# Kernel tuning notes

Hardware: AMD Instinct MI355X
Metric: run time of the kernel (lower is better)

Reference implementation:

```python
import jax, jax.numpy as jnp
import numpy as np

EPS = 1e-12  # torch F.normalize eps
NUM_HEADS = 4
DT = 0.25
NUM_STEPS = 4


def _l2norm(x, axis=-1):
    n = jnp.sqrt(jnp.sum(x * x, axis=axis, keepdims=True))
    return x / jnp.maximum(n, EPS)


def setup_inputs() -> dict:
    key = jax.random.key(0)
    k0, k1, k2, k3, k4 = jax.random.split(key, 5)
    B, T, D = 4, 2048, 256
    z = jax.random.normal(k0, (B, T, D), dtype=jnp.float32)
    omega = jax.random.normal(k1, (1, 1, D), dtype=jnp.float32) * 0.1
    Wqk = jax.random.normal(k2, (2 * D, D), dtype=jnp.float32) * (1.0 / np.sqrt(D))
    Wout = jax.random.normal(k3, (D, D), dtype=jnp.float32) * (1.0 / np.sqrt(D))
    bout = jax.random.normal(k4, (D,), dtype=jnp.float32) * 0.01
    return {"z": z, "omega": omega, "Wqk": Wqk, "Wout": Wout, "bout": bout}


def _kuramoto(x, omega, Wqk, Wout, bout):
    # x: [B, T, D]
    B, T, D = x.shape
    hd = D // NUM_HEADS
    qk = x @ Wqk.T  # [B, T, 2D]
    q, k = jnp.split(qk, 2, axis=-1)
    q = _l2norm(q.reshape(B, T, NUM_HEADS, hd))  # cosine-normalized per head
    k = _l2norm(k.reshape(B, T, NUM_HEADS, hd))
    # coupling: [B, H, T, T] cosine similarity
    coupling = jnp.einsum("bqhd,bkhd->bhqk", q, k)
    # sin nonlinearity replaces softmax
    force = jnp.einsum("bhqk,bkhd->bqhd", jnp.sin(coupling), k).reshape(B, T, D)
    return omega + force @ Wout.T + bout


def reference(z, omega, Wqk, Wout, bout):
    def f(x):
        return _kuramoto(x, omega, Wqk, Wout, bout)

    x = z
    for _ in range(NUM_STEPS):
        x = _l2norm(x)
        k1 = f(x)
        k2 = f(x + DT / 2 * k1)
        k3 = f(x + DT / 2 * k2)
        k4 = f(x + DT * k3)
        x = x + DT / 6 * (k1 + 2 * k2 + 2 * k3 + k4)
    return _l2norm(x)
```

## Files before the change

kernel.cpp:

```cpp
#include <hip/hip_runtime.h>
#include <cmath>

#define NB 4
#define TT 2048
#define DD 256
#define NH 4
#define BT (NB*TT)

static constexpr float DT_ = 0.25f;

typedef _Float16 f16x8 __attribute__((ext_vector_type(8)));
typedef _Float16 f16x4 __attribute__((ext_vector_type(4)));
typedef float    f32x4 __attribute__((ext_vector_type(4)));

static constexpr size_t HSZ = (size_t)NB * NH * TT * 64;
static constexpr size_t FSZ = (size_t)BT * 256;

__device__ __forceinline__ void gload16(const void* g, void* l) {
    __builtin_amdgcn_global_load_lds(
        (const __attribute__((address_space(1))) void*)g,
        (__attribute__((address_space(3))) void*)l,
        16, 0, 0);
}

__global__ __launch_bounds__(256)
void split_weights(const float* __restrict__ Wqk, const float* __restrict__ Wout,
                   _Float16* __restrict__ WqkH, _Float16* __restrict__ WqkL,
                   _Float16* __restrict__ WoutH, _Float16* __restrict__ WoutL)
{
    const int idx = blockIdx.x * 256 + threadIdx.x;
    const float4 v = (idx < 32768) ? ((const float4*)Wqk)[idx]
                                   : ((const float4*)Wout)[idx - 32768];
    f16x4 h, l;
    h[0]=(_Float16)v.x; l[0]=(_Float16)(v.x-(float)h[0]);
    h[1]=(_Float16)v.y; l[1]=(_Float16)(v.y-(float)h[1]);
    h[2]=(_Float16)v.z; l[2]=(_Float16)(v.z-(float)h[2]);
    h[3]=(_Float16)v.w; l[3]=(_Float16)(v.w-(float)h[3]);
    if (idx < 32768) { ((f16x4*)WqkH)[idx] = h; ((f16x4*)WqkL)[idx] = l; }
    else { ((f16x4*)WoutH)[idx-32768] = h; ((f16x4*)WoutL)[idx-32768] = l; }
}

__global__ __launch_bounds__(256)
void comb_weights(const float* __restrict__ Wqk, const float* __restrict__ Wout,
                  const float* __restrict__ omega, const float* __restrict__ bout,
                  _Float16* __restrict__ WcombH, _Float16* __restrict__ WcombL,
                  float* __restrict__ qkob)
{
    __shared__ float qrow[256];
    __shared__ float pr[256];
    const int n = blockIdx.x;
    const int k = threadIdx.x;
    qrow[k] = Wqk[n * 256 + k];
    __syncthreads();
    float s = 0.f;
    for (int m = 0; m < 256; ++m) s = fmaf(qrow[m], Wout[m * 256 + k], s);
    const _Float16 h = (_Float16)s;
    WcombH[n * 256 + k] = h;
    WcombL[n * 256 + k] = (_Float16)(s - (float)h);
    pr[k] = (omega[k] + bout[k]) * qrow[k];
    __syncthreads();
    if (k == 0) {
        float t = 0.f;
        for (int i = 0; i < 256; ++i) t += pr[i];
        qkob[n] = t;
    }
}

__global__ __launch_bounds__(256)
void l2norm_rows(const float* __restrict__ src, float* __restrict__ dst,
                 _Float16* __restrict__ dstH, _Float16* __restrict__ dstL) {
    const int wave = threadIdx.x >> 6;
    const int lane = threadIdx.x & 63;
    const size_t row = (size_t)blockIdx.x * 4 + wave;
    float4 v = ((const float4*)(src + row * DD))[lane];
    float ss = v.x*v.x + v.y*v.y + v.z*v.z + v.w*v.w;
    #pragma unroll
    for (int off = 32; off; off >>= 1) ss += __shfl_xor(ss, off, 64);
    const float inv = 1.0f / fmaxf(sqrtf(ss), 1e-12f);
    v.x *= inv; v.y *= inv; v.z *= inv; v.w *= inv;
    ((float4*)(dst + row * DD))[lane] = v;
    if (dstH != nullptr) {
        f16x4 h, l;
        h[0]=(_Float16)v.x; l[0]=(_Float16)(v.x-(float)h[0]);
        h[1]=(_Float16)v.y; l[1]=(_Float16)(v.y-(float)h[1]);
        h[2]=(_Float16)v.z; l[2]=(_Float16)(v.z-(float)h[2]);
        h[3]=(_Float16)v.w; l[3]=(_Float16)(v.w-(float)h[3]);
        ((f16x4*)(dstH + row * DD))[lane] = h;
        ((f16x4*)(dstL + row * DD))[lane] = l;
    }
}

__global__ __launch_bounds__(256, 2)
void gemm_mfma(const _Float16* __restrict__ AH, const _Float16* __restrict__ AL,
               const _Float16* __restrict__ BH, const _Float16* __restrict__ BL,
               const float* __restrict__ Fp, float* __restrict__ FaccP,
               float* __restrict__ qkx, const float* __restrict__ qkob,
               const float* __restrict__ omega, const float* __restrict__ bout,
               const float* __restrict__ xin, float* __restrict__ xout,
               _Float16* __restrict__ Qhi, _Float16* __restrict__ Qlo,
               _Float16* __restrict__ Khi, _Float16* __restrict__ Klo,
               _Float16* __restrict__ KtrH,
               int mode, float cc, int faccm)
{
    __shared__ _Float16 Ah[128 * 64];
    __shared__ _Float16 Al[128 * 64];
    __shared__ _Float16 Bh[64 * 64];
    __shared__ _Float16 Bl[64 * 64];
    const int m0 = blockIdx.x * 128, n0 = blockIdx.y * 64;
    const int t  = threadIdx.x;
    const int w  = t >> 6;
    const int l  = t & 63;
    const int lr = l & 15;
    const int lq = l >> 4;
    const int m7 = lr & 7;
    const int rr = l >> 3;
    const int lc  = l & 7;
    const int cg  = (lc ^ rr) * 8;
    const int swd = (lc ^ rr) * 8;
    const bool yzero = (blockIdx.y == 0);

    f32x4 acc[2][4];
    #pragma unroll
    for (int s = 0; s < 2; ++s)
        #pragma unroll
        for (int nt = 0; nt < 4; ++nt) acc[s][nt] = (f32x4){0.f,0.f,0.f,0.f};

#define GSTAGE_A(K0) do { \
        _Pragma("unroll") \
        for (int a = 0; a < 4; ++a) { \
            const int rg = 8*w + 32*a; \
            gload16(AH + (size_t)(m0 + rg + rr) * 256 + (K0) + cg, &Ah[rg * 64]); \
            gload16(AL + (size_t)(m0 + rg + rr) * 256 + (K0) + cg, &Al[rg * 64]); \
        } \
    } while (0)

#define GSTAGE_B(K0) do { \
        _Pragma("unroll") \
        for (int a = 0; a < 2; ++a) { \
            const int rg = 8*w + 32*a; \
            gload16(BH + (size_t)(n0 + rg + rr) * 256 + (K0) + cg, &Bh[rg * 64]); \
            gload16(BL + (size_t)(n0 + rg + rr) * 256 + (K0) + cg, &Bl[rg * 64]); \
        } \
    } while (0)

#define FSTAGE(K0) do { \
        _Pragma("unroll") \
        for (int a = 0; a < 4; ++a) { \
            const int row = 8*w + 32*a + rr; \
            const size_t go = (size_t)(m0 + row) * 256 + (K0) + lc * 8; \
            float sv[8]; \
            { const float4 a0 = *(const float4*)(Fp + go); \
              const float4 a1 = *(const float4*)(Fp + go + 4); \
              sv[0]=a0.x; sv[1]=a0.y; sv[2]=a0.z; sv[3]=a0.w; \
              sv[4]=a1.x; sv[5]=a1.y; sv[6]=a1.z; sv[7]=a1.w; } \
            _Pragma("unroll") \
            for (int p = 1; p < 3; ++p) { \
                const float4 a0 = *(const float4*)(Fp + (size_t)p*FSZ + go); \
                const float4 a1 = *(const float4*)(Fp + (size_t)p*FSZ + go + 4); \
                sv[0]+=a0.x; sv[1]+=a0.y; sv[2]+=a0.z; sv[3]+=a0.w; \
                sv[4]+=a1.x; sv[5]+=a1.y; sv[6]+=a1.z; sv[7]+=a1.w; } \
            if (faccm == 3) { \
                const float4 f0 = *(const float4*)(FaccP + go); \
                const float4 f1 = *(const float4*)(FaccP + go + 4); \
                sv[0]+=f0.x; sv[1]+=f0.y; sv[2]+=f0.z; sv[3]+=f0.w; \
                sv[4]+=f1.x; sv[5]+=f1.y; sv[6]+=f1.z; sv[7]+=f1.w; \
            } else if (yzero) { \
                if (faccm == 1) { \
                    *(float4*)(FaccP + go)     = make_float4(sv[0], sv[1], sv[2], sv[3]); \
                    *(float4*)(FaccP + go + 4) = make_float4(sv[4], sv[5], sv[6], sv[7]); \
                } else { \
                    float4 f0 = *(const float4*)(FaccP + go); \
                    float4 f1 = *(const float4*)(FaccP + go + 4); \
                    f0.x += 2.f*sv[0]; f0.y += 2.f*sv[1]; f0.z += 2.f*sv[2]; f0.w += 2.f*sv[3]; \
                    f1.x += 2.f*sv[4]; f1.y += 2.f*sv[5]; f1.z += 2.f*sv[6]; f1.w += 2.f*sv[7]; \
                    *(float4*)(FaccP + go)     = f0; \
                    *(float4*)(FaccP + go + 4) = f1; \
                } \
            } \
            f16x8 hv, lv; \
            _Pragma("unroll") \
            for (int e = 0; e < 8; ++e) { \
                hv[e] = (_Float16)sv[e]; \
                lv[e] = (_Float16)(sv[e] - (float)hv[e]); } \
            *(f16x8*)&Ah[row * 64 + swd] = hv; \
            *(f16x8*)&Al[row * 64 + swd] = lv; \
        } \
    } while (0)

    if (mode == 0) GSTAGE_A(0); else FSTAGE(0);
    GSTAGE_B(0);
    asm volatile("s_waitcnt vmcnt(0) lgkmcnt(0)" ::: "memory");
    __builtin_amdgcn_s_barrier();
    asm volatile("" ::: "memory");

    for (int kc = 0; kc < 4; ++kc) {
        f16x8 ah[2][2], al[2][2], bh[2][4], bl[2][4];
        #pragma unroll
        for (int c = 0; c < 2; ++c) {
            const int xo = (((4*c + lq) ^ m7) << 4);
            #pragma unroll
            for (int s = 0; s < 2; ++s) {
                ah[c][s] = *(const f16x8*)((const char*)Ah + (32*w + 16*s + lr) * 128 + xo);
                al[c][s] = *(const f16x8*)((const char*)Al + (32*w + 16*s + lr) * 128 + xo);
            }
            #pragma unroll
            for (int nt = 0; nt < 4; ++nt) {
                bh[c][nt] = *(const f16x8*)((const char*)Bh + (16*nt + lr) * 128 + xo);
                bl[c][nt] = *(const f16x8*)((const char*)Bl + (16*nt + lr) * 128 + xo);
            }
        }
        asm volatile("s_waitcnt lgkmcnt(0)" ::: "memory");
        __builtin_amdgcn_s_barrier();
        asm volatile("" ::: "memory");
        if (kc < 3) {
            GSTAGE_B((kc + 1) * 64);
            if (mode == 0) GSTAGE_A((kc + 1) * 64); else FSTAGE((kc + 1) * 64);
        }
        #pragma unroll
        for (int c = 0; c < 2; ++c)
            #pragma unroll
            for (int s = 0; s < 2; ++s)
                #pragma unroll
                for (int nt = 0; nt < 4; ++nt) {
                    acc[s][nt] = __builtin_amdgcn_mfma_f32_16x16x32_f16(ah[c][s], bh[c][nt], acc[s][nt], 0, 0, 0);
                    acc[s][nt] = __builtin_amdgcn_mfma_f32_16x16x32_f16(ah[c][s], bl[c][nt], acc[s][nt], 0, 0, 0);
                    acc[s][nt] = __builtin_amdgcn_mfma_f32_16x16x32_f16(al[c][s], bh[c][nt], acc[s][nt], 0, 0, 0);
                }
        if (kc < 3) asm volatile("s_waitcnt vmcnt(0) lgkmcnt(0)" ::: "memory");
        __builtin_amdgcn_s_barrier();
        asm volatile("" ::: "memory");
    }
#undef GSTAGE_A
#undef GSTAGE_B
#undef FSTAGE

    if (mode == 2) {
        #pragma unroll
        for (int s = 0; s < 2; ++s) {
            const int row0 = m0 + 32*w + 16*s + 4*lq;
            #pragma unroll
            for (int nt = 0; nt < 4; ++nt) {
                const int col = n0 + 16*nt + lr;
                const float ob = omega[col] + bout[col];
                #pragma unroll
                for (int r = 0; r < 4; ++r) {
                    const size_t off = (size_t)(row0 + r) * 256 + col;
                    xout[off] = xin[off] + (DT_ / 6.0f) * acc[s][nt][r] + DT_ * ob;
                }
            }
        }
    } else {
        float val[2][4][4];
        #pragma unroll
        for (int s = 0; s < 2; ++s) {
            const int row0 = m0 + 32*w + 16*s + 4*lq;
            #pragma unroll
            for (int nt = 0; nt < 4; ++nt) {
                const int col = n0 + 16*nt + lr;
                #pragma unroll
                for (int r = 0; r < 4; ++r) {
                    const size_t qo = (size_t)(row0 + r) * 512 + col;
                    if (mode == 0) {
                        val[s][nt][r] = acc[s][nt][r];
                        qkx[qo] = acc[s][nt][r];
                    } else {
                        val[s][nt][r] = qkx[qo] + cc * (acc[s][nt][r] + qkob[col]);
                    }
                }
            }
        }
        float ss[2][4];
        #pragma unroll
        for (int s = 0; s < 2; ++s)
            #pragma unroll
            for (int r = 0; r < 4; ++r) {
                float v = 0.f;
                #pragma unroll
                for (int nt = 0; nt < 4; ++nt) v += val[s][nt][r] * val[s][nt][r];
                ss[s][r] = v;
            }
        #pragma unroll
        for (int off = 1; off < 16; off <<= 1)
            #pragma unroll
            for (int s = 0; s < 2; ++s)
                #pragma unroll
                for (int r = 0; r < 4; ++r)
                    ss[s][r] += __shfl_xor(ss[s][r], off, 64);
        const int  b    = m0 >> 11;
        const int  h    = (n0 >> 6) & 3;
        const bool is_k = (n0 >= 256);
        const size_t bhi = (size_t)b * NH + h;
        _Float16* dhi = (is_k ? Khi : Qhi) + bhi * (size_t)TT * 64;
        _Float16* dlo = (is_k ? Klo : Qlo) + bhi * (size_t)TT * 64;
        const int mloc = m0 & (TT - 1);
        _Float16* Pt = Ah;
        #pragma unroll
        for (int s = 0; s < 2; ++s) {
            const int r0 = 32*w + 16*s + 4*lq;
            float inv[4];
            #pragma unroll
            for (int r = 0; r < 4; ++r) inv[r] = 1.0f / fmaxf(sqrtf(ss[s][r]), 1e-12f);
            #pragma unroll
            for (int nt = 0; nt < 4; ++nt) {
                const int d = 16*nt + lr;
                f16x4 hv, lv;
                #pragma unroll
                for (int r = 0; r < 4; ++r) {
                    const float v2 = val[s][nt][r] * inv[r];
                    hv[r] = (_Float16)v2;
                    lv[r] = (_Float16)(v2 - (float)hv[r]);
                    dhi[(size_t)(mloc + r0 + r) * 64 + d] = hv[r];
                    dlo[(size_t)(mloc + r0 + r) * 64 + d] = lv[r];
                }
                if (is_k) {
                    *(f16x4*)((char*)Pt + d * 256 + ((r0 * 2) ^ ((d & 7) << 4))) = hv;
                }
            }
        }
        if (is_k) {
            __syncthreads();
            const size_t kb = bhi * (size_t)64 * TT + mloc;
            #pragma unroll
            for (int p = 0; p < 4; ++p) {
                const int d   = (t >> 4) + 16 * p;
                const int lm0 = (t & 15) * 8;
                f16x8 v = *(const f16x8*)((const char*)Pt + d * 256 + ((lm0 * 2) ^ ((d & 7) << 4)));
                *(f16x8*)(KtrH + kb + (size_t)d * TT + lm0) = v;
            }
        }
    }
}

__global__ __launch_bounds__(256, 3)
void kuramoto_attn(const _Float16* __restrict__ Qhi, const _Float16* __restrict__ Qlo,
                   const _Float16* __restrict__ Khi, const _Float16* __restrict__ Klo,
                   const _Float16* __restrict__ KtrH,
                   float* __restrict__ Fp)
{
    __shared__ _Float16 KjH[64 * 64];
    __shared__ _Float16 KjL[64 * 64];
    __shared__ _Float16 KdH[64 * 64];
    __shared__ _Float16 Pw[4][2][16 * 64];
    const int bh = blockIdx.x;
    const int b  = bh >> 2, h = bh & 3;
    const size_t base  = (size_t)bh * TT * 64;
    const size_t tbase = (size_t)bh * 64 * TT;
    const int t0 = blockIdx.y * 11;
    const int tn = (blockIdx.y == 2) ? 10 : 11;
    float* Fout = Fp + (size_t)blockIdx.y * FSZ;
    const int t = threadIdx.x;
    const int w = t >> 6;
    const int l = t & 63;
    const int lr = l & 15;
    const int lq = l >> 4;
    const int i0 = blockIdx.z * 128 + w * 32;
    const int m7 = lr & 7;
    const int x0 = ((lq ^ m7) << 4);
    const int x1 = (((lq + 4) ^ m7) << 4);
    const int rr = l >> 3;
    const int lc8 = (l & 7) * 8;
    const int sw = ((l & 7) ^ rr) * 8;
    const int rg = 8 * w + rr;

    f16x8 qh[2][2], ql[2][2];
    #pragma unroll
    for (int s = 0; s < 2; ++s) {
        const size_t qoff = base + (size_t)(i0 + 16*s + lr) * 64 + lq * 8;
        qh[s][0] = *(const f16x8*)(Qhi + qoff);
        qh[s][1] = *(const f16x8*)(Qhi + qoff + 32);
        ql[s][0] = *(const f16x8*)(Qlo + qoff);
        ql[s][1] = *(const f16x8*)(Qlo + qoff + 32);
    }

    f32x4 Facc[2][4];
    #pragma unroll
    for (int s = 0; s < 2; ++s)
        #pragma unroll
        for (int nt = 0; nt < 4; ++nt) Facc[s][nt] = (f32x4){0.f, 0.f, 0.f, 0.f};

    uint4 gA0, gA1, gB0, gB1, gC0, gC1;
#define GLOAD(TTi) do { \
        const int j0_ = (t0 + (TTi)) * 64; \
        gA0 = *(const uint4*)(Khi  + base  + (size_t)(j0_ + rg)      * 64 + lc8); \
        gA1 = *(const uint4*)(Khi  + base  + (size_t)(j0_ + rg + 32) * 64 + lc8); \
        gB0 = *(const uint4*)(Klo  + base  + (size_t)(j0_ + rg)      * 64 + lc8); \
        gB1 = *(const uint4*)(Klo  + base  + (size_t)(j0_ + rg + 32) * 64 + lc8); \
        gC0 = *(const uint4*)(KtrH + tbase + (size_t)rg        * TT + j0_ + lc8); \
        gC1 = *(const uint4*)(KtrH + tbase + (size_t)(rg + 32) * TT + j0_ + lc8); \
    } while (0)

    GLOAD(0);

    for (int tt = 0; tt < tn; ++tt) {
        *(uint4*)&KjH[rg * 64 + sw]        = gA0;
        *(uint4*)&KjH[(rg + 32) * 64 + sw] = gA1;
        *(uint4*)&KjL[rg * 64 + sw]        = gB0;
        *(uint4*)&KjL[(rg + 32) * 64 + sw] = gB1;
        *(uint4*)&KdH[rg * 64 + sw]        = gC0;
        *(uint4*)&KdH[(rg + 32) * 64 + sw] = gC1;
        if (tt + 1 < tn) GLOAD(tt + 1);
        asm volatile("s_waitcnt lgkmcnt(0)" ::: "memory");
        __builtin_amdgcn_s_barrier();
        asm volatile("" ::: "memory");

        #pragma unroll
        for (int nt = 0; nt < 4; ++nt) {
            const int rb = (16*nt + lr) * 128;
            f16x8 kh0 = *(const f16x8*)((const char*)KjH + rb + x0);
            f16x8 kh1 = *(const f16x8*)((const char*)KjH + rb + x1);
            f16x8 kl0 = *(const f16x8*)((const char*)KjL + rb + x0);
            f16x8 kl1 = *(const f16x8*)((const char*)KjL + rb + x1);
            #pragma unroll
            for (int s = 0; s < 2; ++s) {
                f32x4 a = (f32x4){0.f, 0.f, 0.f, 0.f};
                __builtin_amdgcn_s_setprio(1);
                a = __builtin_amdgcn_mfma_f32_16x16x32_f16(kh0, qh[s][0], a, 0, 0, 0);
                a = __builtin_amdgcn_mfma_f32_16x16x32_f16(kh1, qh[s][1], a, 0, 0, 0);
                a = __builtin_amdgcn_mfma_f32_16x16x32_f16(kl0, qh[s][0], a, 0, 0, 0);
                a = __builtin_amdgcn_mfma_f32_16x16x32_f16(kl1, qh[s][1], a, 0, 0, 0);
                a = __builtin_amdgcn_mfma_f32_16x16x32_f16(kh0, ql[s][0], a, 0, 0, 0);
                a = __builtin_amdgcn_mfma_f32_16x16x32_f16(kh1, ql[s][1], a, 0, 0, 0);
                __builtin_amdgcn_s_setprio(0);
                f16x4 pv;
                #pragma unroll
                for (int r = 0; r < 4; ++r) pv[r] = (_Float16)__sinf(a[r]);
                *(f16x4*)((char*)&Pw[w][0][0] + s * 2048 + lr * 128
                          + (((2*nt + (lq >> 1)) ^ m7) << 4) + ((lq & 1) << 3)) = pv;
            }
        }
        f16x8 ph[2][2];
        #pragma unroll
        for (int s = 0; s < 2; ++s) {
            ph[s][0] = *(const f16x8*)((const char*)&Pw[w][0][0] + s * 2048 + lr * 128 + x0);
            ph[s][1] = *(const f16x8*)((const char*)&Pw[w][0][0] + s * 2048 + lr * 128 + x1);
        }
        #pragma unroll
        for (int nt = 0; nt < 4; ++nt) {
            const int rb = (16*nt + lr) * 128;
            f16x8 kh0 = *(const f16x8*)((const char*)KdH + rb + x0);
            f16x8 kh1 = *(const f16x8*)((const char*)KdH + rb + x1);
            __builtin_amdgcn_s_setprio(1);
            #pragma unroll
            for (int s = 0; s < 2; ++s) {
                Facc[s][nt] = __builtin_amdgcn_mfma_f32_16x16x32_f16(ph[s][0], kh0, Facc[s][nt], 0, 0, 0);
                Facc[s][nt] = __builtin_amdgcn_mfma_f32_16x16x32_f16(ph[s][1], kh1, Facc[s][nt], 0, 0, 0);
            }
            __builtin_amdgcn_s_setprio(0);
        }
        __builtin_amdgcn_s_barrier();
        asm volatile("" ::: "memory");
    }
#undef GLOAD

    #pragma unroll
    for (int s = 0; s < 2; ++s) {
        float* fo = Fout + ((size_t)b * TT + i0 + 16*s + 4*lq) * 256 + h * 64 + lr;
        #pragma unroll
        for (int nt = 0; nt < 4; ++nt)
            #pragma unroll
            for (int r = 0; r < 4; ++r)
                fo[(size_t)r * 256 + nt * 16] = Facc[s][nt][r];
    }
}

extern "C" void kernel_launch(void* const* d_in, const int* in_sizes, int n_in,
                              void* d_out, int out_size, void* d_ws, size_t ws_size,
                              hipStream_t stream) {
    const float* z     = (const float*)d_in[0];
    const float* omega = (const float*)d_in[1];
    const float* Wqk   = (const float*)d_in[2];
    const float* Wout  = (const float*)d_in[3];
    const float* bout  = (const float*)d_in[4];

    float* x    = (float*)d_ws;
    float* Facc = x + FSZ;
    float* Fp   = Facc + FSZ;
    float* qkx  = Fp + 3 * FSZ;
    float* qkob = qkx + (size_t)BT * 512;
    _Float16* xsH  = (_Float16*)(qkob + 512);
    _Float16* xsL  = xsH  + FSZ;
    _Float16* Qhi  = xsL  + FSZ;
    _Float16* Qlo  = Qhi  + HSZ;
    _Float16* Khi  = Qlo  + HSZ;
    _Float16* Klo  = Khi  + HSZ;
    _Float16* KtrH = Klo  + HSZ;
    _Float16* WqkH = KtrH + HSZ;
    _Float16* WqkL = WqkH + (size_t)512 * 256;
    _Float16* WoutH= WqkL + (size_t)512 * 256;
    _Float16* WoutL= WoutH + (size_t)256 * 256;
    _Float16* WcombH = WoutL + (size_t)256 * 256;
    _Float16* WcombL = WcombH + (size_t)512 * 256;

    split_weights<<<192, 256, 0, stream>>>(Wqk, Wout, WqkH, WqkL, WoutH, WoutL);
    comb_weights<<<512, 256, 0, stream>>>(Wqk, Wout, omega, bout, WcombH, WcombL, qkob);

    for (int step = 0; step < 4; ++step) {
        l2norm_rows<<<BT / 4, 256, 0, stream>>>(step == 0 ? z : x, x, xsH, xsL);
        gemm_mfma<<<dim3(BT / 128, 8), 256, 0, stream>>>(
            xsH, xsL, WqkH, WqkL, nullptr, nullptr, qkx, nullptr,
            nullptr, nullptr, nullptr, nullptr,
            Qhi, Qlo, Khi, Klo, KtrH, 0, 0.f, 0);
        kuramoto_attn<<<dim3(NB * NH, 3, TT / 128), 256, 0, stream>>>(
            Qhi, Qlo, Khi, Klo, KtrH, Fp);
        for (int s = 1; s <= 3; ++s) {
            const float cs = (s == 3) ? 0.25f : 0.125f;
            gemm_mfma<<<dim3(BT / 128, 8), 256, 0, stream>>>(
                nullptr, nullptr, WcombH, WcombL, Fp, Facc, qkx, qkob,
                nullptr, nullptr, nullptr, nullptr,
                Qhi, Qlo, Khi, Klo, KtrH, 1, cs, (s == 1) ? 1 : 2);
            kuramoto_attn<<<dim3(NB * NH, 3, TT / 128), 256, 0, stream>>>(
                Qhi, Qlo, Khi, Klo, KtrH, Fp);
        }
        gemm_mfma<<<dim3(BT / 128, 4), 256, 0, stream>>>(
            nullptr, nullptr, WoutH, WoutL, Fp, Facc, nullptr, nullptr,
            omega, bout, x, x,
            nullptr, nullptr, nullptr, nullptr, nullptr, 2, 0.f, 3);
    }
    l2norm_rows<<<BT / 4, 256, 0, stream>>>(x, (float*)d_out, nullptr, nullptr);
}
```

Baseline: 1.158 ms.

## Switch attention MFMAs to 32x32x16 and keep sin(P) in registers

Rewrites the coupling and force matmuls in the attention kernel to use 32x32x16 MFMA tiles instead of 16x16x32. The 32x32 output layout is arranged so the sin-activated coupling tile can feed the second MFMA directly from registers, which removes the per-wave Pw LDS staging buffer with its stores and reloads. The trade-offs are larger accumulators per lane, which adds register pressure against the launch bound of three blocks, and K^T LDS reads now assembled from two 4-element halves.

After: 1.170 ms. No clear change (+1.0%).

```diff
diff --git a/kernel.cpp b/kernel.cpp
--- a/kernel.cpp
+++ b/kernel.cpp
@@ -12,6 +12,7 @@
 typedef _Float16 f16x8 __attribute__((ext_vector_type(8)));
 typedef _Float16 f16x4 __attribute__((ext_vector_type(4)));
 typedef float    f32x4 __attribute__((ext_vector_type(4)));
+typedef float    f32x16 __attribute__((ext_vector_type(16)));
 
 static constexpr size_t HSZ = (size_t)NB * NH * TT * 64;
 static constexpr size_t FSZ = (size_t)BT * 256;
@@ -340,7 +341,6 @@
     __shared__ _Float16 KjH[64 * 64];
     __shared__ _Float16 KjL[64 * 64];
     __shared__ _Float16 KdH[64 * 64];
-    __shared__ _Float16 Pw[4][2][16 * 64];
     const int bh = blockIdx.x;
     const int b  = bh >> 2, h = bh & 3;
     const size_t base  = (size_t)bh * TT * 64;
@@ -351,32 +351,28 @@
     const int t = threadIdx.x;
     const int w = t >> 6;
     const int l = t & 63;
-    const int lr = l & 15;
-    const int lq = l >> 4;
+    const int il = l & 31;
+    const int h5 = l >> 5;
     const int i0 = blockIdx.z * 128 + w * 32;
-    const int m7 = lr & 7;
-    const int x0 = ((lq ^ m7) << 4);
-    const int x1 = (((lq + 4) ^ m7) << 4);
+    const int s7 = il & 7;
     const int rr = l >> 3;
     const int lc8 = (l & 7) * 8;
     const int sw = ((l & 7) ^ rr) * 8;
     const int rg = 8 * w + rr;
 
-    f16x8 qh[2][2], ql[2][2];
+    f16x8 qh[4], ql[4];
     #pragma unroll
-    for (int s = 0; s < 2; ++s) {
-        const size_t qoff = base + (size_t)(i0 + 16*s + lr) * 64 + lq * 8;
-        qh[s][0] = *(const f16x8*)(Qhi + qoff);
-        qh[s][1] = *(const f16x8*)(Qhi + qoff + 32);
-        ql[s][0] = *(const f16x8*)(Qlo + qoff);
-        ql[s][1] = *(const f16x8*)(Qlo + qoff + 32);
-    }
-
-    f32x4 Facc[2][4];
+    for (int kc = 0; kc < 4; ++kc) {
+        const size_t qoff = base + (size_t)(i0 + il) * 64 + 16*kc + 8*h5;
+        qh[kc] = *(const f16x8*)(Qhi + qoff);
+        ql[kc] = *(const f16x8*)(Qlo + qoff);
+    }
+
+    f32x16 Fac[2];
     #pragma unroll
-    for (int s = 0; s < 2; ++s)
-        #pragma unroll
-        for (int nt = 0; nt < 4; ++nt) Facc[s][nt] = (f32x4){0.f, 0.f, 0.f, 0.f};
+    for (int db = 0; db < 2; ++db)
+        #pragma unroll
+        for (int r = 0; r < 16; ++r) Fac[db][r] = 0.f;
 
     uint4 gA0, gA1, gB0, gB1, gC0, gC1;
 #define GLOAD(TTi) do { \
@@ -403,48 +399,50 @@
         __builtin_amdgcn_s_barrier();
         asm volatile("" ::: "memory");
 
-        #pragma unroll
-        for (int nt = 0; nt < 4; ++nt) {
-            const int rb = (16*nt + lr) * 128;
-            f16x8 kh0 = *(const f16x8*)((const char*)KjH + rb + x0);
-            f16x8 kh1 = *(const f16x8*)((const char*)KjH + rb + x1);
-            f16x8 kl0 = *(const f16x8*)((const char*)KjL + rb + x0);
-            f16x8 kl1 = *(const f16x8*)((const char*)KjL + rb + x1);
-            #pragma unroll
-            for (int s = 0; s < 2; ++s) {
-                f32x4 a = (f32x4){0.f, 0.f, 0.f, 0.f};
-                __builtin_amdgcn_s_setprio(1);
-                a = __builtin_amdgcn_mfma_f32_16x16x32_f16(kh0, qh[s][0], a, 0, 0, 0);
-                a = __builtin_amdgcn_mfma_f32_16x16x32_f16(kh1, qh[s][1], a, 0, 0, 0);
-                a = __builtin_amdgcn_mfma_f32_16x16x32_f16(kl0, qh[s][0], a, 0, 0, 0);
-                a = __builtin_amdgcn_mfma_f32_16x16x32_f16(kl1, qh[s][1], a, 0, 0, 0);
-                a = __builtin_amdgcn_mfma_f32_16x16x32_f16(kh0, ql[s][0], a, 0, 0, 0);
-                a = __builtin_amdgcn_mfma_f32_16x16x32_f16(kh1, ql[s][1], a, 0, 0, 0);
-                __builtin_amdgcn_s_setprio(0);
-                f16x4 pv;
-                #pragma unroll
-                for (int r = 0; r < 4; ++r) pv[r] = (_Float16)__sinf(a[r]);
-                *(f16x4*)((char*)&Pw[w][0][0] + s * 2048 + lr * 128
-                          + (((2*nt + (lq >> 1)) ^ m7) << 4) + ((lq & 1) << 3)) = pv;
-            }
-        }
         f16x8 ph[2][2];
         #pragma unroll
-        for (int s = 0; s < 2; ++s) {
-            ph[s][0] = *(const f16x8*)((const char*)&Pw[w][0][0] + s * 2048 + lr * 128 + x0);
-            ph[s][1] = *(const f16x8*)((const char*)&Pw[w][0][0] + s * 2048 + lr * 128 + x1);
-        }
-        #pragma unroll
-        for (int nt = 0; nt < 4; ++nt) {
-            const int rb = (16*nt + lr) * 128;
-            f16x8 kh0 = *(const f16x8*)((const char*)KdH + rb + x0);
-            f16x8 kh1 = *(const f16x8*)((const char*)KdH + rb + x1);
+        for (int jb = 0; jb < 2; ++jb) {
+            f32x16 sacc;
+            #pragma unroll
+            for (int r = 0; r < 16; ++r) sacc[r] = 0.f;
+            const int rowb = (32*jb + il) * 128;
             __builtin_amdgcn_s_setprio(1);
             #pragma unroll
-            for (int s = 0; s < 2; ++s) {
-                Facc[s][nt] = __builtin_amdgcn_mfma_f32_16x16x32_f16(ph[s][0], kh0, Facc[s][nt], 0, 0, 0);
-                Facc[s][nt] = __builtin_amdgcn_mfma_f32_16x16x32_f16(ph[s][1], kh1, Facc[s][nt], 0, 0, 0);
-            }
+            for (int kc = 0; kc < 4; ++kc) {
+                const int ch = (((2*kc + h5) ^ s7) << 4);
+                f16x8 khA = *(const f16x8*)((const char*)KjH + rowb + ch);
+                f16x8 klA = *(const f16x8*)((const char*)KjL + rowb + ch);
+                sacc = __builtin_amdgcn_mfma_f32_32x32x16_f16(khA, qh[kc], sacc, 0, 0, 0);
+                sacc = __builtin_amdgcn_mfma_f32_32x32x16_f16(klA, qh[kc], sacc, 0, 0, 0);
+                sacc = __builtin_amdgcn_mfma_f32_32x32x16_f16(khA, ql[kc], sacc, 0, 0, 0);
+            }
+            __builtin_amdgcn_s_setprio(0);
+            f16x8 v0, v1;
+            #pragma unroll
+            for (int e = 0; e < 8; ++e) {
+                v0[e] = (_Float16)__sinf(sacc[e]);
+                v1[e] = (_Float16)__sinf(sacc[8 + e]);
+            }
+            ph[jb][0] = v0;
+            ph[jb][1] = v1;
+        }
+
+        #pragma unroll
+        for (int db = 0; db < 2; ++db) {
+            const int rowd = (il + 32*db) * 128;
+            __builtin_amdgcn_s_setprio(1);
+            #pragma unroll
+            for (int jb = 0; jb < 2; ++jb)
+                #pragma unroll
+                for (int cp = 0; cp < 2; ++cp) {
+                    const int q1 = 4*jb + 2*cp;
+                    f16x4 klo = *(const f16x4*)((const char*)KdH + rowd + ((q1 ^ s7) << 4) + 8*h5);
+                    f16x4 khi = *(const f16x4*)((const char*)KdH + rowd + (((q1 + 1) ^ s7) << 4) + 8*h5);
+                    f16x8 kf;
+                    #pragma unroll
+                    for (int e = 0; e < 4; ++e) { kf[e] = klo[e]; kf[4 + e] = khi[e]; }
+                    Fac[db] = __builtin_amdgcn_mfma_f32_32x32x16_f16(ph[jb][cp], kf, Fac[db], 0, 0, 0);
+                }
             __builtin_amdgcn_s_setprio(0);
         }
         __builtin_amdgcn_s_barrier();
@@ -453,14 +451,12 @@
 #undef GLOAD
 
     #pragma unroll
-    for (int s = 0; s < 2; ++s) {
-        float* fo = Fout + ((size_t)b * TT + i0 + 16*s + 4*lq) * 256 + h * 64 + lr;
-        #pragma unroll
-        for (int nt = 0; nt < 4; ++nt)
-            #pragma unroll
-            for (int r = 0; r < 4; ++r)
-                fo[(size_t)r * 256 + nt * 16] = Facc[s][nt][r];
-    }
+    for (int db = 0; db < 2; ++db)
+        #pragma unroll
+        for (int r = 0; r < 16; ++r) {
+            const int irow = (r & 3) + 8 * (r >> 2) + 4 * h5;
+            Fout[((size_t)b * TT + i0 + irow) * 256 + h * 64 + il + 32 * db] = Fac[db][r];
+        }
 }
 
 extern "C" void kernel_launch(void* const* d_in, const int* in_sizes, int n_in,
```
